# Performance work log

Measured on AMD Instinct MI355X. Metric: run time of the kernel, lower is better.

## Reference

```python
import jax, jax.numpy as jnp
import numpy as np

D_MODEL = 1024
NUM_HEADS = 16
D_K = D_MODEL // NUM_HEADS


def setup_inputs() -> dict:
    key = jax.random.key(0)
    ks = jax.random.split(key, 5)
    sd = np.sqrt(2.0 / (D_MODEL + D_MODEL))
    x = jax.random.normal(ks[0], (2, 2048, D_MODEL), dtype=jnp.float32)
    # weights stored as [out_features, in_features] like torch Linear
    w_q = jax.random.normal(ks[1], (D_MODEL, D_MODEL), dtype=jnp.float32) * (sd * sd)
    w_k = jax.random.normal(ks[2], (D_MODEL, D_MODEL), dtype=jnp.float32) * (sd * sd)
    w_v = jax.random.normal(ks[3], (D_MODEL, D_MODEL), dtype=jnp.float32) * (sd * sd)
    w_o = jax.random.normal(ks[4], (D_MODEL, D_MODEL), dtype=jnp.float32) * (sd * sd)
    return {"x": x, "w_q": w_q, "w_k": w_k, "w_v": w_v, "w_o": w_o}


def reference(x, w_q, w_k, w_v, w_o):
    B, S, D = x.shape
    H, Dk = NUM_HEADS, D_K
    # projections: x @ W.T
    q = (x @ w_q.T).reshape(B, S, H, Dk).transpose(0, 2, 1, 3)  # [B,H,S,Dk]
    k = (x @ w_k.T).reshape(B, S, H, Dk).transpose(0, 2, 1, 3)
    v = (x @ w_v.T).reshape(B, S, H, Dk).transpose(0, 2, 1, 3)
    scale = 1.0 / np.sqrt(Dk).astype(np.float32)
    scores = jnp.einsum('bhqd,bhkd->bhqk', q, k) * scale  # [B,H,S,S]
    causal = jnp.tril(jnp.ones((S, S), dtype=bool))
    scores = jnp.where(causal, scores, -jnp.inf)
    weights = jax.nn.softmax(scores, axis=-1)
    attn = jnp.einsum('bhqk,bhkd->bhqd', weights, v)  # [B,H,S,Dk]
    attn = attn.transpose(0, 2, 1, 3).reshape(B, S, D)
    return attn @ w_o.T
```

## Files before the change

kernel.cpp:

```cpp
#include <hip/hip_runtime.h>

typedef __attribute__((ext_vector_type(8))) short short8;
typedef __attribute__((ext_vector_type(4))) float f32x4;
typedef __attribute__((ext_vector_type(16))) float f32x16;
typedef __attribute__((ext_vector_type(2))) unsigned int u32x2;

#define DM 1024
#define SL 2048
#define NH 16
#define DKH 64
#define NB 2

__device__ __forceinline__ unsigned short f2bf(float f) {
    union { float f; unsigned int u; } a; a.f = f;
    unsigned int r = a.u + 0x7FFFu + ((a.u >> 16) & 1u);
    return (unsigned short)(r >> 16);
}

__device__ __forceinline__ void gl_lds16(const void* g, void* l) {
    __builtin_amdgcn_global_load_lds(
        (__attribute__((address_space(1))) void*)(g),
        (__attribute__((address_space(3))) void*)(l), 16, 0, 0);
}

__device__ __forceinline__ unsigned int cvtpk_bf16(float lo, float hi) {
    unsigned int r;
    asm("v_cvt_pk_bf16_f32 %0, %1, %2" : "=v"(r) : "v"(lo), "v"(hi));
    return r;
}

__device__ __forceinline__ void pl32swap(unsigned int &a, unsigned int &b) {
    u32x2 r = __builtin_amdgcn_permlane32_swap(a, b, false, false);
    a = r[0]; b = r[1];
}
__device__ __forceinline__ void pl32swapf(float &a, float &b) {
    unsigned int ua = __float_as_uint(a), ub = __float_as_uint(b);
    pl32swap(ua, ub);
    a = __uint_as_float(ua); b = __uint_as_float(ub);
}

__global__ __launch_bounds__(256) void convert_kernel(
    const float* __restrict__ x,  const float* __restrict__ wq,
    const float* __restrict__ wk, const float* __restrict__ wv,
    const float* __restrict__ wo,
    unsigned short* __restrict__ xb,  unsigned short* __restrict__ wqb,
    unsigned short* __restrict__ wkb, unsigned short* __restrict__ wvb,
    unsigned short* __restrict__ wob)
{
    const int NX = NB * SL * DM;
    const int NW = DM * DM;
    int t4 = (blockIdx.x * 256 + threadIdx.x) * 4;
    const float* src; unsigned short* dst; int off; float scale = 1.0f;
    if (t4 < NX)              { src = x;  dst = xb;  off = t4; }
    else if (t4 < NX + NW)    { src = wq; dst = wqb; off = t4 - NX; scale = 0.125f * 1.44269504088896f; }
    else if (t4 < NX + 2*NW)  { src = wk; dst = wkb; off = t4 - NX - NW; }
    else if (t4 < NX + 3*NW)  { src = wv; dst = wvb; off = t4 - NX - 2*NW; }
    else                      { src = wo; dst = wob; off = t4 - NX - 3*NW; }
    float4 v = *(const float4*)(src + off);
    unsigned long long p =
        (unsigned long long)f2bf(v.x * scale)
      | ((unsigned long long)f2bf(v.y * scale) << 16)
      | ((unsigned long long)f2bf(v.z * scale) << 32)
      | ((unsigned long long)f2bf(v.w * scale) << 48);
    *(unsigned long long*)(dst + off) = p;
}

__global__ __launch_bounds__(256) void gemm_bt(
    const unsigned short* __restrict__ A,
    const unsigned short* __restrict__ Bw,
    unsigned short* __restrict__ oq, unsigned short* __restrict__ ok,
    unsigned short* __restrict__ ov)
{
    __shared__ __align__(16) unsigned short As[128 * 64];
    __shared__ __align__(16) unsigned short Bs[128 * 64];
    const int tid  = threadIdx.x;
    const int lane = tid & 63;
    const int wave = tid >> 6;
    const int wm = (wave >> 1) * 64, wn = (wave & 1) * 64;
    const int bx = blockIdx.x, by = blockIdx.y;
    const int c    = lane & 15;
    const int kg16 = (lane >> 4) * 16;
    const int swz  = (c & 7) << 4;

    f32x4 acc[4][4];
    #pragma unroll
    for (int i = 0; i < 4; i++)
        #pragma unroll
        for (int j = 0; j < 4; j++) acc[i][j] = (f32x4){0.f, 0.f, 0.f, 0.f};

    const char* Ab = (const char*)A  + by * 128 * (DM * 2);
    const char* Bb = (const char*)Bw + bx * 128 * (DM * 2);

    for (int k0 = 0; k0 < DM; k0 += 64) {
        #pragma unroll
        for (int i = 0; i < 4; i++) {
            int o  = i * 4096 + tid * 16;
            int r  = o >> 7;
            int cb = o & 127;
            int src = r * (DM * 2) + k0 * 2 + (cb ^ ((r & 7) << 4));
            gl_lds16(Ab + src, (char*)As + o);
            gl_lds16(Bb + src, (char*)Bs + o);
        }
        __syncthreads();
        #pragma unroll
        for (int kk = 0; kk < 2; kk++) {
            short8 a[4], bfr[4];
            #pragma unroll
            for (int mi = 0; mi < 4; mi++)
                a[mi] = *(const short8*)((const char*)As
                        + (wm + mi * 16 + c) * 128 + ((kk * 64 + kg16) ^ swz));
            #pragma unroll
            for (int ni = 0; ni < 4; ni++)
                bfr[ni] = *(const short8*)((const char*)Bs
                        + (wn + ni * 16 + c) * 128 + ((kk * 64 + kg16) ^ swz));
            #pragma unroll
            for (int mi = 0; mi < 4; mi++)
                #pragma unroll
                for (int ni = 0; ni < 4; ni++)
                    acc[mi][ni] = __builtin_amdgcn_mfma_f32_16x16x32_bf16(
                        a[mi], bfr[ni], acc[mi][ni], 0, 0, 0);
        }
        __syncthreads();
    }

    const int r4 = (lane >> 4) * 4;
    const int mat = (bx * 128) >> 10;
    unsigned short* outb = (mat == 0) ? oq : (mat == 1) ? ok : ov;
    const int nb = bx * 128 - (mat << 10);
    #pragma unroll
    for (int mi = 0; mi < 4; mi++) {
        int m_g = by * 128 + wm + mi * 16 + r4;
        int b_  = m_g >> 11, s_ = m_g & 2047;
        #pragma unroll
        for (int ni = 0; ni < 4; ni++) {
            int n_l = nb + wn + ni * 16 + c;
            int h = n_l >> 6, dk = n_l & 63;
            #pragma unroll
            for (int j = 0; j < 4; j++)
                outb[((b_ * NH + h) * SL + (s_ + j)) * DKH + dk] = f2bf(acc[mi][ni][j]);
        }
    }
}

__global__ __launch_bounds__(256) void gemm_o(
    const unsigned short* __restrict__ A,
    const unsigned short* __restrict__ Bw,
    float* __restrict__ of)
{
    __shared__ __align__(16) unsigned short As[64 * 64];
    __shared__ __align__(16) unsigned short Bs[128 * 64];
    const int tid  = threadIdx.x;
    const int lane = tid & 63;
    const int wave = tid >> 6;
    const int wm = (wave >> 1) * 32, wn = (wave & 1) * 64;
    const int bx = blockIdx.x, by = blockIdx.y;
    const int c    = lane & 15;
    const int kg16 = (lane >> 4) * 16;
    const int swz  = (c & 7) << 4;

    f32x4 acc[2][4];
    #pragma unroll
    for (int i = 0; i < 2; i++)
        #pragma unroll
        for (int j = 0; j < 4; j++) acc[i][j] = (f32x4){0.f, 0.f, 0.f, 0.f};

    const char* Ab = (const char*)A  + by * 64  * (DM * 2);
    const char* Bb = (const char*)Bw + bx * 128 * (DM * 2);

    for (int k0 = 0; k0 < DM; k0 += 64) {
        #pragma unroll
        for (int i = 0; i < 2; i++) {
            int o  = i * 4096 + tid * 16;
            int r  = o >> 7, cb = o & 127;
            int src = r * (DM * 2) + k0 * 2 + (cb ^ ((r & 7) << 4));
            gl_lds16(Ab + src, (char*)As + o);
        }
        #pragma unroll
        for (int i = 0; i < 4; i++) {
            int o  = i * 4096 + tid * 16;
            int r  = o >> 7, cb = o & 127;
            int src = r * (DM * 2) + k0 * 2 + (cb ^ ((r & 7) << 4));
            gl_lds16(Bb + src, (char*)Bs + o);
        }
        __syncthreads();
        #pragma unroll
        for (int kk = 0; kk < 2; kk++) {
            short8 a[2], bfr[4];
            #pragma unroll
            for (int mi = 0; mi < 2; mi++)
                a[mi] = *(const short8*)((const char*)As
                        + (wm + mi * 16 + c) * 128 + ((kk * 64 + kg16) ^ swz));
            #pragma unroll
            for (int ni = 0; ni < 4; ni++)
                bfr[ni] = *(const short8*)((const char*)Bs
                        + (wn + ni * 16 + c) * 128 + ((kk * 64 + kg16) ^ swz));
            #pragma unroll
            for (int mi = 0; mi < 2; mi++)
                #pragma unroll
                for (int ni = 0; ni < 4; ni++)
                    acc[mi][ni] = __builtin_amdgcn_mfma_f32_16x16x32_bf16(
                        a[mi], bfr[ni], acc[mi][ni], 0, 0, 0);
        }
        __syncthreads();
    }

    const int r4 = (lane >> 4) * 4;
    #pragma unroll
    for (int mi = 0; mi < 2; mi++) {
        int m_g = by * 64 + wm + mi * 16 + r4;
        #pragma unroll
        for (int ni = 0; ni < 4; ni++) {
            int n_g = bx * 128 + wn + ni * 16 + c;
            #pragma unroll
            for (int j = 0; j < 4; j++)
                of[(m_g + j) * DM + n_g] = acc[mi][ni][j];
        }
    }
}

__global__ __launch_bounds__(128) void attn_kernel(
    const unsigned short* __restrict__ Q,
    const unsigned short* __restrict__ K,
    const unsigned short* __restrict__ V,
    unsigned short* __restrict__ O,
    unsigned short* __restrict__ partO,
    float* __restrict__ ml)
{
    __shared__ __align__(16) unsigned short Kl[64 * 64];
    __shared__ __align__(16) unsigned short Vt[8 * 64 * 8];
    const int tid = threadIdx.x, lane = tid & 63, wave = tid >> 6;
    const int ln31 = lane & 31, hi = lane >> 5;
    const int m  = blockIdx.x >> 5;
    const int bh = blockIdx.x & 31;
    const int rr = m >> 3, g = m & 7;
    int item;
    if (rr < 2)       item = m;
    else if (rr == 2) item = 16 + g;
    else if (rr == 3) item = 31 - g;
    else if (rr == 4) item = 32 + g;
    else              item = 47 - g;
    int qt, cch, t0, ntc;
    if (item < 16)      { qt = 16 + item;              cch = 0; t0 = 0;  ntc = 16; }
    else if (item < 32) { int j = item - 16; qt = 31 - j; cch = 1; t0 = 16; ntc = 16 - j; }
    else                { int j = item - 32; qt = 15 - j; cch = 0; t0 = 0;  ntc = 16 - j; }
    const int b = bh >> 4, h = bh & 15;
    const int bhi = b * NH + h;
    const unsigned short* Qg = Q + bhi * (SL * DKH);
    const unsigned short* Kg = K + bhi * (SL * DKH);
    const unsigned short* Vg = V + bhi * (SL * DKH);
    const int qw = qt * 64 + wave * 32;
    const int vd0 = (tid & 31) * 2, c0 = tid >> 5;

    short8 qf[4];
    #pragma unroll
    for (int ks = 0; ks < 4; ks++)
        qf[ks] = *(const short8*)&Qg[(qw + ln31) * DKH + ks * 16 + hi * 8];

    f32x16 OT0, OT1;
    #pragma unroll
    for (int r = 0; r < 16; r++) { OT0[r] = 0.f; OT1[r] = 0.f; }
    float mrun = -1e30f, ls = 0.f;

    short8 kreg[4];
    unsigned int vreg[16];


    {
        const size_t kvb = (size_t)t0 * 64;
        #pragma unroll
        for (int i = 0; i < 4; i++) {
            int s = i * 128 + tid;
            int kv = s >> 3, k8 = s & 7;
            kreg[i] = *(const short8*)&Kg[(kvb + kv) * DKH + k8 * 8];
        }
        #pragma unroll
        for (int c2 = 0; c2 < 2; c2++)
            #pragma unroll
            for (int i = 0; i < 8; i++)
                vreg[c2 * 8 + i] = *(const unsigned int*)&Vg[(kvb + (c0 + 4 * c2) * 8 + i) * DKH + vd0];
        #pragma unroll
        for (int i = 0; i < 4; i++) {
            int s = i * 128 + tid;
            int kv = s >> 3, k8 = (s & 7) ^ (kv & 7);
            *(short8*)((char*)Kl + kv * 128 + k8 * 16) = kreg[i];
        }
        #pragma unroll
        for (int c2 = 0; c2 < 2; c2++) {
            int chunk = c0 + 4 * c2;
            short8 sa, sb;
            #pragma unroll
            for (int i = 0; i < 8; i++) {
                unsigned int pr = vreg[c2 * 8 + i];
                sa[i] = (short)(pr & 0xFFFFu);
                sb[i] = (short)(pr >> 16);
            }
            *(short8*)&Vt[(chunk * 64 + vd0) * 8]     = sa;
            *(short8*)&Vt[(chunk * 64 + vd0 + 1) * 8] = sb;
        }
        __syncthreads();
    }

    for (int tt = 0; tt < ntc; ++tt) {
        const int t = t0 + tt;
        const int kv0 = t * 64;

        if (tt + 1 < ntc) {
            const size_t kv1 = (size_t)(t + 1) * 64;
            #pragma unroll
            for (int i = 0; i < 4; i++) {
                int s = i * 128 + tid;
                int kv = s >> 3, k8 = s & 7;
                kreg[i] = *(const short8*)&Kg[(kv1 + kv) * DKH + k8 * 8];
            }
            #pragma unroll
            for (int c2 = 0; c2 < 2; c2++)
                #pragma unroll
                for (int i = 0; i < 8; i++)
                    vreg[c2 * 8 + i] = *(const unsigned int*)&Vg[(kv1 + (c0 + 4 * c2) * 8 + i) * DKH + vd0];
        }

        f32x16 S0, S1;
        #pragma unroll
        for (int r = 0; r < 16; r++) { S0[r] = 0.f; S1[r] = 0.f; }
        __builtin_amdgcn_s_setprio(1);
        #pragma unroll
        for (int ks = 0; ks < 4; ks++) {
            int ko = (ks * 32 + hi * 16) ^ ((ln31 & 7) << 4);
            short8 ka0 = *(const short8*)((const char*)Kl + ln31 * 128 + ko);
            short8 ka1 = *(const short8*)((const char*)Kl + (32 + ln31) * 128 + ko);
            S0 = __builtin_amdgcn_mfma_f32_32x32x16_bf16(ka0, qf[ks], S0, 0, 0, 0);
            S1 = __builtin_amdgcn_mfma_f32_32x32x16_bf16(ka1, qf[ks], S1, 0, 0, 0);
        }
        __builtin_amdgcn_s_setprio(0);

        if (t == qt) {
            const int qrel0 = qw + ln31 - kv0 - 4 * hi;
            const int qrel1 = qrel0 - 32;
            #pragma unroll
            for (int r = 0; r < 16; r++) {
                const int ro = (r & 3) + 8 * (r >> 2);
                if (ro > qrel0) S0[r] = -1e30f;
                if (ro > qrel1) S1[r] = -1e30f;
            }
        }

        float mx = fmaxf(S0[0], S1[0]);
        #pragma unroll
        for (int r = 1; r < 16; r++) mx = fmaxf(mx, fmaxf(S0[r], S1[r]));
        float ma = mx, mb = mx;
        pl32swapf(ma, mb);
        float rm = fmaxf(ma, mb);

        if (__any(rm > mrun + 8.f)) {
            float nm = fmaxf(mrun, rm);
            float corr = __builtin_amdgcn_exp2f(mrun - nm);
            mrun = nm; ls *= corr;
            #pragma unroll
            for (int r = 0; r < 16; r++) { OT0[r] *= corr; OT1[r] *= corr; }
        }

        float psum = 0.f;
        #pragma unroll
        for (int r = 0; r < 16; r++) {
            S0[r] = __builtin_amdgcn_exp2f(S0[r] - mrun); psum += S0[r];
            S1[r] = __builtin_amdgcn_exp2f(S1[r] - mrun); psum += S1[r];
        }
        ls += psum;

        short8 pf[4];
        {
            unsigned int wa, wb, wc, wd;
            wa = cvtpk_bf16(S0[0], S0[1]);   wb = cvtpk_bf16(S0[4], S0[5]);
            pl32swap(wa, wb);
            wc = cvtpk_bf16(S0[2], S0[3]);   wd = cvtpk_bf16(S0[6], S0[7]);
            pl32swap(wc, wd);
            union { unsigned int u[4]; short8 s; } w0 = {{wa, wc, wb, wd}};
            pf[0] = w0.s;

            wa = cvtpk_bf16(S0[8], S0[9]);   wb = cvtpk_bf16(S0[12], S0[13]);
            pl32swap(wa, wb);
            wc = cvtpk_bf16(S0[10], S0[11]); wd = cvtpk_bf16(S0[14], S0[15]);
            pl32swap(wc, wd);
            union { unsigned int u[4]; short8 s; } w1 = {{wa, wc, wb, wd}};
            pf[1] = w1.s;

            wa = cvtpk_bf16(S1[0], S1[1]);   wb = cvtpk_bf16(S1[4], S1[5]);
            pl32swap(wa, wb);
            wc = cvtpk_bf16(S1[2], S1[3]);   wd = cvtpk_bf16(S1[6], S1[7]);
            pl32swap(wc, wd);
            union { unsigned int u[4]; short8 s; } w2 = {{wa, wc, wb, wd}};
            pf[2] = w2.s;

            wa = cvtpk_bf16(S1[8], S1[9]);   wb = cvtpk_bf16(S1[12], S1[13]);
            pl32swap(wa, wb);
            wc = cvtpk_bf16(S1[10], S1[11]); wd = cvtpk_bf16(S1[14], S1[15]);
            pl32swap(wc, wd);
            union { unsigned int u[4]; short8 s; } w3 = {{wa, wc, wb, wd}};
            pf[3] = w3.s;
        }

        __builtin_amdgcn_s_setprio(1);
        #pragma unroll
        for (int ks2 = 0; ks2 < 4; ks2++) {
            int slot = (ks2 * 2 + hi) * 64;
            short8 va0 = *(const short8*)&Vt[(slot + ln31) * 8];
            short8 va1 = *(const short8*)&Vt[(slot + 32 + ln31) * 8];
            OT0 = __builtin_amdgcn_mfma_f32_32x32x16_bf16(va0, pf[ks2], OT0, 0, 0, 0);
            OT1 = __builtin_amdgcn_mfma_f32_32x32x16_bf16(va1, pf[ks2], OT1, 0, 0, 0);
        }
        __builtin_amdgcn_s_setprio(0);

        if (tt + 1 < ntc) {
            __syncthreads();
            #pragma unroll
            for (int i = 0; i < 4; i++) {
                int s = i * 128 + tid;
                int kv = s >> 3, k8 = (s & 7) ^ (kv & 7);
                *(short8*)((char*)Kl + kv * 128 + k8 * 16) = kreg[i];
            }
            #pragma unroll
            for (int c2 = 0; c2 < 2; c2++) {
                int chunk = c0 + 4 * c2;
                short8 sa, sb;
                #pragma unroll
                for (int i = 0; i < 8; i++) {
                    unsigned int pr = vreg[c2 * 8 + i];
                    sa[i] = (short)(pr & 0xFFFFu);
                    sb[i] = (short)(pr >> 16);
                }
                *(short8*)&Vt[(chunk * 64 + vd0) * 8]     = sa;
                *(short8*)&Vt[(chunk * 64 + vd0 + 1) * 8] = sb;
            }
            __syncthreads();
        }
    }

    float la = ls, lb = ls;
    pl32swapf(la, lb);
    const float lrow = la + lb;
    const int qrow_l = wave * 32 + ln31;
    if (qt >= 16) {
        const int rec = (bh * 16 + (qt - 16)) * 2 + cch;
        unsigned short* po = partO + (size_t)rec * 4096;
        if (hi == 0) {
            ml[(rec * 64 + qrow_l) * 2]     = mrun;
            ml[(rec * 64 + qrow_l) * 2 + 1] = lrow;
        }
        #pragma unroll
        for (int r = 0; r < 16; r++) {
            const int d0 = (r & 3) + 8 * (r >> 2) + 4 * hi;
            po[qrow_l * 64 + d0]      = f2bf(OT0[r]);
            po[qrow_l * 64 + 32 + d0] = f2bf(OT1[r]);
        }
    } else {
        float inv = 1.0f / lrow;
        const int qrow = qw + ln31;
        const size_t base = (size_t)(b * SL + qrow) * DM + h * DKH;
        #pragma unroll
        for (int r = 0; r < 16; r++) {
            const int d0 = (r & 3) + 8 * (r >> 2) + 4 * hi;
            O[base + d0]      = f2bf(OT0[r] * inv);
            O[base + 32 + d0] = f2bf(OT1[r] * inv);
        }
    }
}

__global__ __launch_bounds__(256) void combine_kernel(
    const unsigned short* __restrict__ partO,
    const float* __restrict__ ml,
    unsigned short* __restrict__ O)
{
    const int gi = blockIdx.x * 8 + (threadIdx.x >> 5);
    const int ln = threadIdx.x & 31;
    const int bh = gi >> 10, rem = gi & 1023;
    const int qtl = rem >> 6, row = rem & 63;
    const int qt = 16 + qtl;
    const int rec0 = (bh * 16 + qtl) * 2;
    const float m0 = ml[(rec0 * 64 + row) * 2];
    const float l0 = ml[(rec0 * 64 + row) * 2 + 1];
    const float m1 = ml[((rec0 + 1) * 64 + row) * 2];
    const float l1 = ml[((rec0 + 1) * 64 + row) * 2 + 1];
    const float M  = fmaxf(m0, m1);
    const float w0 = exp2f(m0 - M), w1 = exp2f(m1 - M);
    const float inv = 1.0f / (w0 * l0 + w1 * l1);
    const unsigned int u0 = *(const unsigned int*)&partO[(size_t)rec0 * 4096 + row * 64 + ln * 2];
    const unsigned int u1 = *(const unsigned int*)&partO[(size_t)(rec0 + 1) * 4096 + row * 64 + ln * 2];
    const float a0 = __uint_as_float(u0 << 16);
    const float b0 = __uint_as_float(u0 & 0xFFFF0000u);
    const float a1 = __uint_as_float(u1 << 16);
    const float b1 = __uint_as_float(u1 & 0xFFFF0000u);
    const float oa = (a0 * w0 + a1 * w1) * inv;
    const float ob = (b0 * w0 + b1 * w1) * inv;
    const unsigned int pack = (unsigned int)f2bf(oa) | ((unsigned int)f2bf(ob) << 16);
    const int b = bh >> 4, h = bh & 15;
    const size_t base = (size_t)(b * SL + qt * 64 + row) * DM + h * DKH;
    *(unsigned int*)&O[base + ln * 2] = pack;
}

extern "C" void kernel_launch(void* const* d_in, const int* in_sizes, int n_in,
                              void* d_out, int out_size, void* d_ws, size_t ws_size,
                              hipStream_t stream)
{
    const float* x  = (const float*)d_in[0];
    const float* wq = (const float*)d_in[1];
    const float* wk = (const float*)d_in[2];
    const float* wv = (const float*)d_in[3];
    const float* wo = (const float*)d_in[4];
    char* ws = (char*)d_ws;
    unsigned short* xb  = (unsigned short*)(ws);
    unsigned short* wqb = (unsigned short*)(ws + (8ll  << 20));
    unsigned short* wkb = (unsigned short*)(ws + (10ll << 20));
    unsigned short* wvb = (unsigned short*)(ws + (12ll << 20));
    unsigned short* wob = (unsigned short*)(ws + (14ll << 20));
    unsigned short* Qb  = (unsigned short*)(ws + (16ll << 20));
    unsigned short* Kb  = (unsigned short*)(ws + (24ll << 20));
    unsigned short* Vb  = (unsigned short*)(ws + (32ll << 20));
    unsigned short* Abf = (unsigned short*)(ws + (40ll << 20));
    unsigned short* partO = (unsigned short*)(ws);
    float*          mlbuf = (float*)(ws + (8ll << 20));
    float* out = (float*)d_out;

    convert_kernel<<<dim3(8192), dim3(256), 0, stream>>>(
        x, wq, wk, wv, wo, xb, wqb, wkb, wvb, wob);

    gemm_bt<<<dim3(24, 32), dim3(256), 0, stream>>>(xb, wqb, Qb, Kb, Vb);

    attn_kernel<<<dim3(1536), dim3(128), 0, stream>>>(Qb, Kb, Vb, Abf, partO, mlbuf);
    combine_kernel<<<dim3(4096), dim3(256), 0, stream>>>(partO, mlbuf, Abf);

    gemm_o<<<dim3(8, 64), dim3(256), 0, stream>>>(Abf, wob, out);
}
```

Baseline: 110.3 us.

## Use persistent atomic work queue for attention with finer causal splits and double-buffered K/V

```diff
diff --git a/kernel.cpp b/kernel.cpp
--- a/kernel.cpp
+++ b/kernel.cpp
@@ -10,6 +10,7 @@
 #define NH 16
 #define DKH 64
 #define NB 2
+#define NITEMS 1792
 
 __device__ __forceinline__ unsigned short f2bf(float f) {
     union { float f; unsigned int u; } a; a.f = f;
@@ -69,8 +70,9 @@
     const unsigned short* __restrict__ A,
     const unsigned short* __restrict__ Bw,
     unsigned short* __restrict__ oq, unsigned short* __restrict__ ok,
-    unsigned short* __restrict__ ov)
+    unsigned short* __restrict__ ov, unsigned int* __restrict__ counter)
 {
+    if (blockIdx.x == 0 && blockIdx.y == 0 && threadIdx.x == 0) *counter = 0u;
     __shared__ __align__(16) unsigned short As[128 * 64];
     __shared__ __align__(16) unsigned short Bs[128 * 64];
     const int tid  = threadIdx.x;
@@ -224,200 +226,72 @@
     const unsigned short* __restrict__ V,
     unsigned short* __restrict__ O,
     unsigned short* __restrict__ partO,
-    float* __restrict__ ml)
+    float* __restrict__ ml,
+    unsigned int* __restrict__ counter)
 {
-    __shared__ __align__(16) unsigned short Kl[64 * 64];
-    __shared__ __align__(16) unsigned short Vt[8 * 64 * 8];
+    __shared__ __align__(16) unsigned short Kl[2][64 * 64];
+    __shared__ __align__(16) unsigned short Vt[2][8 * 64 * 8];
+    __shared__ int s_item;
     const int tid = threadIdx.x, lane = tid & 63, wave = tid >> 6;
     const int ln31 = lane & 31, hi = lane >> 5;
-    const int m  = blockIdx.x >> 5;
-    const int bh = blockIdx.x & 31;
-    const int rr = m >> 3, g = m & 7;
-    int item;
-    if (rr < 2)       item = m;
-    else if (rr == 2) item = 16 + g;
-    else if (rr == 3) item = 31 - g;
-    else if (rr == 4) item = 32 + g;
-    else              item = 47 - g;
-    int qt, cch, t0, ntc;
-    if (item < 16)      { qt = 16 + item;              cch = 0; t0 = 0;  ntc = 16; }
-    else if (item < 32) { int j = item - 16; qt = 31 - j; cch = 1; t0 = 16; ntc = 16 - j; }
-    else                { int j = item - 32; qt = 15 - j; cch = 0; t0 = 0;  ntc = 16 - j; }
-    const int b = bh >> 4, h = bh & 15;
-    const int bhi = b * NH + h;
-    const unsigned short* Qg = Q + bhi * (SL * DKH);
-    const unsigned short* Kg = K + bhi * (SL * DKH);
-    const unsigned short* Vg = V + bhi * (SL * DKH);
-    const int qw = qt * 64 + wave * 32;
     const int vd0 = (tid & 31) * 2, c0 = tid >> 5;
 
-    short8 qf[4];
-    #pragma unroll
-    for (int ks = 0; ks < 4; ks++)
-        qf[ks] = *(const short8*)&Qg[(qw + ln31) * DKH + ks * 16 + hi * 8];
-
-    f32x16 OT0, OT1;
-    #pragma unroll
-    for (int r = 0; r < 16; r++) { OT0[r] = 0.f; OT1[r] = 0.f; }
-    float mrun = -1e30f, ls = 0.f;
-
-    short8 kreg[4];
-    unsigned int vreg[16];
-
-
-    {
-        const size_t kvb = (size_t)t0 * 64;
-        #pragma unroll
-        for (int i = 0; i < 4; i++) {
-            int s = i * 128 + tid;
-            int kv = s >> 3, k8 = s & 7;
-            kreg[i] = *(const short8*)&Kg[(kvb + kv) * DKH + k8 * 8];
-        }
-        #pragma unroll
-        for (int c2 = 0; c2 < 2; c2++)
-            #pragma unroll
-            for (int i = 0; i < 8; i++)
-                vreg[c2 * 8 + i] = *(const unsigned int*)&Vg[(kvb + (c0 + 4 * c2) * 8 + i) * DKH + vd0];
-        #pragma unroll
-        for (int i = 0; i < 4; i++) {
-            int s = i * 128 + tid;
-            int kv = s >> 3, k8 = (s & 7) ^ (kv & 7);
-            *(short8*)((char*)Kl + kv * 128 + k8 * 16) = kreg[i];
-        }
-        #pragma unroll
-        for (int c2 = 0; c2 < 2; c2++) {
-            int chunk = c0 + 4 * c2;
-            short8 sa, sb;
-            #pragma unroll
-            for (int i = 0; i < 8; i++) {
-                unsigned int pr = vreg[c2 * 8 + i];
-                sa[i] = (short)(pr & 0xFFFFu);
-                sb[i] = (short)(pr >> 16);
-            }
-            *(short8*)&Vt[(chunk * 64 + vd0) * 8]     = sa;
-            *(short8*)&Vt[(chunk * 64 + vd0 + 1) * 8] = sb;
-        }
+    for (;;) {
+        if (tid == 0) s_item = (int)atomicAdd(counter, 1u);
         __syncthreads();
-    }
-
-    for (int tt = 0; tt < ntc; ++tt) {
-        const int t = t0 + tt;
-        const int kv0 = t * 64;
-
-        if (tt + 1 < ntc) {
-            const size_t kv1 = (size_t)(t + 1) * 64;
+        const int it = s_item;
+        if (it >= NITEMS) break;
+
+        const int bh = it & 31;
+        const int w  = it >> 5;
+        int qt, t0, ntc, cch;
+        if (w < 48) {
+            qt = 31 - (w >> 1); cch = w & 1;
+            const int h0 = (qt + 2) >> 1;
+            t0 = cch ? h0 : 0; ntc = cch ? (qt + 1 - h0) : h0;
+        } else {
+            qt = 55 - w; cch = 0; t0 = 0; ntc = qt + 1;
+        }
+        const int b = bh >> 4, h = bh & 15;
+        const int bhi = b * NH + h;
+        const unsigned short* Qg = Q + bhi * (SL * DKH);
+        const unsigned short* Kg = K + bhi * (SL * DKH);
+        const unsigned short* Vg = V + bhi * (SL * DKH);
+        const int qw = qt * 64 + wave * 32;
+
+        short8 qf[4];
+        #pragma unroll
+        for (int ks = 0; ks < 4; ks++)
+            qf[ks] = *(const short8*)&Qg[(qw + ln31) * DKH + ks * 16 + hi * 8];
+
+        f32x16 OT0, OT1;
+        #pragma unroll
+        for (int r = 0; r < 16; r++) { OT0[r] = 0.f; OT1[r] = 0.f; }
+        float mrun = -1e30f, ls = 0.f;
+
+        unsigned int vreg[16];
+
+        {
+            const size_t kvb = (size_t)t0 * 64;
             #pragma unroll
             for (int i = 0; i < 4; i++) {
                 int s = i * 128 + tid;
-                int kv = s >> 3, k8 = s & 7;
-                kreg[i] = *(const short8*)&Kg[(kv1 + kv) * DKH + k8 * 8];
+                int kv = s >> 3;
+                int k8 = (s & 7) ^ (kv & 7);
+                gl_lds16((const char*)Kg + (kvb + kv) * 128 + k8 * 16,
+                         (char*)&Kl[0][0] + s * 16);
             }
             #pragma unroll
             for (int c2 = 0; c2 < 2; c2++)
                 #pragma unroll
                 for (int i = 0; i < 8; i++)
-                    vreg[c2 * 8 + i] = *(const unsigned int*)&Vg[(kv1 + (c0 + 4 * c2) * 8 + i) * DKH + vd0];
-        }
-
-        f32x16 S0, S1;
-        #pragma unroll
-        for (int r = 0; r < 16; r++) { S0[r] = 0.f; S1[r] = 0.f; }
-        __builtin_amdgcn_s_setprio(1);
-        #pragma unroll
-        for (int ks = 0; ks < 4; ks++) {
-            int ko = (ks * 32 + hi * 16) ^ ((ln31 & 7) << 4);
-            short8 ka0 = *(const short8*)((const char*)Kl + ln31 * 128 + ko);
-            short8 ka1 = *(const short8*)((const char*)Kl + (32 + ln31) * 128 + ko);
-            S0 = __builtin_amdgcn_mfma_f32_32x32x16_bf16(ka0, qf[ks], S0, 0, 0, 0);
-            S1 = __builtin_amdgcn_mfma_f32_32x32x16_bf16(ka1, qf[ks], S1, 0, 0, 0);
-        }
-        __builtin_amdgcn_s_setprio(0);
-
-        if (t == qt) {
-            const int qrel0 = qw + ln31 - kv0 - 4 * hi;
-            const int qrel1 = qrel0 - 32;
-            #pragma unroll
-            for (int r = 0; r < 16; r++) {
-                const int ro = (r & 3) + 8 * (r >> 2);
-                if (ro > qrel0) S0[r] = -1e30f;
-                if (ro > qrel1) S1[r] = -1e30f;
-            }
-        }
-
-        float mx = fmaxf(S0[0], S1[0]);
-        #pragma unroll
-        for (int r = 1; r < 16; r++) mx = fmaxf(mx, fmaxf(S0[r], S1[r]));
-        float ma = mx, mb = mx;
-        pl32swapf(ma, mb);
-        float rm = fmaxf(ma, mb);
-
-        if (__any(rm > mrun + 8.f)) {
-            float nm = fmaxf(mrun, rm);
-            float corr = __builtin_amdgcn_exp2f(mrun - nm);
-            mrun = nm; ls *= corr;
-            #pragma unroll
-            for (int r = 0; r < 16; r++) { OT0[r] *= corr; OT1[r] *= corr; }
-        }
-
-        float psum = 0.f;
-        #pragma unroll
-        for (int r = 0; r < 16; r++) {
-            S0[r] = __builtin_amdgcn_exp2f(S0[r] - mrun); psum += S0[r];
-            S1[r] = __builtin_amdgcn_exp2f(S1[r] - mrun); psum += S1[r];
-        }
-        ls += psum;
-
-        short8 pf[4];
-        {
-            unsigned int wa, wb, wc, wd;
-            wa = cvtpk_bf16(S0[0], S0[1]);   wb = cvtpk_bf16(S0[4], S0[5]);
-            pl32swap(wa, wb);
-            wc = cvtpk_bf16(S0[2], S0[3]);   wd = cvtpk_bf16(S0[6], S0[7]);
-            pl32swap(wc, wd);
-            union { unsigned int u[4]; short8 s; } w0 = {{wa, wc, wb, wd}};
-            pf[0] = w0.s;
-
-            wa = cvtpk_bf16(S0[8], S0[9]);   wb = cvtpk_bf16(S0[12], S0[13]);
-            pl32swap(wa, wb);
-            wc = cvtpk_bf16(S0[10], S0[11]); wd = cvtpk_bf16(S0[14], S0[15]);
-            pl32swap(wc, wd);
-            union { unsigned int u[4]; short8 s; } w1 = {{wa, wc, wb, wd}};
-            pf[1] = w1.s;
-
-            wa = cvtpk_bf16(S1[0], S1[1]);   wb = cvtpk_bf16(S1[4], S1[5]);
-            pl32swap(wa, wb);
-            wc = cvtpk_bf16(S1[2], S1[3]);   wd = cvtpk_bf16(S1[6], S1[7]);
-            pl32swap(wc, wd);
-            union { unsigned int u[4]; short8 s; } w2 = {{wa, wc, wb, wd}};
-            pf[2] = w2.s;
-
-            wa = cvtpk_bf16(S1[8], S1[9]);   wb = cvtpk_bf16(S1[12], S1[13]);
-            pl32swap(wa, wb);
-            wc = cvtpk_bf16(S1[10], S1[11]); wd = cvtpk_bf16(S1[14], S1[15]);
-            pl32swap(wc, wd);
-            union { unsigned int u[4]; short8 s; } w3 = {{wa, wc, wb, wd}};
-            pf[3] = w3.s;
-        }
-
-        __builtin_amdgcn_s_setprio(1);
-        #pragma unroll
-        for (int ks2 = 0; ks2 < 4; ks2++) {
-            int slot = (ks2 * 2 + hi) * 64;
-            short8 va0 = *(const short8*)&Vt[(slot + ln31) * 8];
-            short8 va1 = *(const short8*)&Vt[(slot + 32 + ln31) * 8];
-            OT0 = __builtin_amdgcn_mfma_f32_32x32x16_bf16(va0, pf[ks2], OT0, 0, 0, 0);
-            OT1 = __builtin_amdgcn_mfma_f32_32x32x16_bf16(va1, pf[ks2], OT1, 0, 0, 0);
-        }
-        __builtin_amdgcn_s_setprio(0);
-
-        if (tt + 1 < ntc) {
-            __syncthreads();
-            #pragma unroll
-            for (int i = 0; i < 4; i++) {
-                int s = i * 128 + tid;
-                int kv = s >> 3, k8 = (s & 7) ^ (kv & 7);
-                *(short8*)((char*)Kl + kv * 128 + k8 * 16) = kreg[i];
-            }
+                    vreg[c2 * 8 + i] = *(const unsigned int*)&Vg[(kvb + (c0 + 4 * c2) * 8 + i) * DKH + vd0];
+        }
+
+        for (int tt = 0; tt < ntc; ++tt) {
+            const int t = t0 + tt;
+            const int buf = tt & 1;
+            const int kv0 = t * 64;
             #pragma unroll
             for (int c2 = 0; c2 < 2; c2++) {
                 int chunk = c0 + 4 * c2;
@@ -428,39 +302,159 @@
                     sa[i] = (short)(pr & 0xFFFFu);
                     sb[i] = (short)(pr >> 16);
                 }
-                *(short8*)&Vt[(chunk * 64 + vd0) * 8]     = sa;
-                *(short8*)&Vt[(chunk * 64 + vd0 + 1) * 8] = sb;
+                *(short8*)&Vt[buf][(chunk * 64 + vd0) * 8]     = sa;
+                *(short8*)&Vt[buf][(chunk * 64 + vd0 + 1) * 8] = sb;
             }
             __syncthreads();
-        }
-    }
-
-    float la = ls, lb = ls;
-    pl32swapf(la, lb);
-    const float lrow = la + lb;
-    const int qrow_l = wave * 32 + ln31;
-    if (qt >= 16) {
-        const int rec = (bh * 16 + (qt - 16)) * 2 + cch;
-        unsigned short* po = partO + (size_t)rec * 4096;
-        if (hi == 0) {
-            ml[(rec * 64 + qrow_l) * 2]     = mrun;
-            ml[(rec * 64 + qrow_l) * 2 + 1] = lrow;
-        }
-        #pragma unroll
-        for (int r = 0; r < 16; r++) {
-            const int d0 = (r & 3) + 8 * (r >> 2) + 4 * hi;
-            po[qrow_l * 64 + d0]      = f2bf(OT0[r]);
-            po[qrow_l * 64 + 32 + d0] = f2bf(OT1[r]);
-        }
-    } else {
-        float inv = 1.0f / lrow;
-        const int qrow = qw + ln31;
-        const size_t base = (size_t)(b * SL + qrow) * DM + h * DKH;
-        #pragma unroll
-        for (int r = 0; r < 16; r++) {
-            const int d0 = (r & 3) + 8 * (r >> 2) + 4 * hi;
-            O[base + d0]      = f2bf(OT0[r] * inv);
-            O[base + 32 + d0] = f2bf(OT1[r] * inv);
+
+            if (tt + 1 < ntc) {
+                const size_t kv1 = (size_t)(t + 1) * 64;
+                #pragma unroll
+                for (int i = 0; i < 4; i++) {
+                    int s = i * 128 + tid;
+                    int kv = s >> 3;
+                    int k8 = (s & 7) ^ (kv & 7);
+                    gl_lds16((const char*)Kg + (kv1 + kv) * 128 + k8 * 16,
+                             (char*)&Kl[buf ^ 1][0] + s * 16);
+                }
+                #pragma unroll
+                for (int c2 = 0; c2 < 2; c2++)
+                    #pragma unroll
+                    for (int i = 0; i < 8; i++)
+                        vreg[c2 * 8 + i] = *(const unsigned int*)&Vg[(kv1 + (c0 + 4 * c2) * 8 + i) * DKH + vd0];
+            }
+
+            const char* kb = (const char*)&Kl[buf][0];
+            const unsigned short* vb = &Vt[buf][0];
+
+            f32x16 S0, S1;
+            #pragma unroll
+            for (int r = 0; r < 16; r++) { S0[r] = 0.f; S1[r] = 0.f; }
+            __builtin_amdgcn_s_setprio(1);
+            #pragma unroll
+            for (int ks = 0; ks < 4; ks++) {
+                int ko = (ks * 32 + hi * 16) ^ ((ln31 & 7) << 4);
+                short8 ka0 = *(const short8*)(kb + ln31 * 128 + ko);
+                short8 ka1 = *(const short8*)(kb + (32 + ln31) * 128 + ko);
+                S0 = __builtin_amdgcn_mfma_f32_32x32x16_bf16(ka0, qf[ks], S0, 0, 0, 0);
+                S1 = __builtin_amdgcn_mfma_f32_32x32x16_bf16(ka1, qf[ks], S1, 0, 0, 0);
+            }
+            __builtin_amdgcn_s_setprio(0);
+
+            if (t == qt) {
+                const int qrel0 = qw + ln31 - kv0 - 4 * hi;
+                const int qrel1 = qrel0 - 32;
+                #pragma unroll
+                for (int r = 0; r < 16; r++) {
+                    const int ro = (r & 3) + 8 * (r >> 2);
+                    if (ro > qrel0) S0[r] = -1e30f;
+                    if (ro > qrel1) S1[r] = -1e30f;
+                }
+            }
+
+            float mt[8];
+            #pragma unroll
+            for (int r = 0; r < 8; r++)
+                mt[r] = fmaxf(fmaxf(S0[r], S0[r + 8]), fmaxf(S1[r], S1[r + 8]));
+            float mx = fmaxf(fmaxf(fmaxf(mt[0], mt[1]), fmaxf(mt[2], mt[3])),
+                             fmaxf(fmaxf(mt[4], mt[5]), fmaxf(mt[6], mt[7])));
+            float ma = mx, mb = mx;
+            pl32swapf(ma, mb);
+            float rm = fmaxf(ma, mb);
+
+            if (__any(rm > mrun + 8.f)) {
+                float nm = fmaxf(mrun, rm);
+                float corr = __builtin_amdgcn_exp2f(mrun - nm);
+                mrun = nm; ls *= corr;
+                #pragma unroll
+                for (int r = 0; r < 16; r++) { OT0[r] *= corr; OT1[r] *= corr; }
+            }
+
+            float ps0 = 0.f, ps1 = 0.f, ps2 = 0.f, ps3 = 0.f;
+            #pragma unroll
+            for (int r = 0; r < 16; r += 4) {
+                S0[r]     = __builtin_amdgcn_exp2f(S0[r]     - mrun); ps0 += S0[r];
+                S0[r + 1] = __builtin_amdgcn_exp2f(S0[r + 1] - mrun); ps1 += S0[r + 1];
+                S0[r + 2] = __builtin_amdgcn_exp2f(S0[r + 2] - mrun); ps2 += S0[r + 2];
+                S0[r + 3] = __builtin_amdgcn_exp2f(S0[r + 3] - mrun); ps3 += S0[r + 3];
+                S1[r]     = __builtin_amdgcn_exp2f(S1[r]     - mrun); ps0 += S1[r];
+                S1[r + 1] = __builtin_amdgcn_exp2f(S1[r + 1] - mrun); ps1 += S1[r + 1];
+                S1[r + 2] = __builtin_amdgcn_exp2f(S1[r + 2] - mrun); ps2 += S1[r + 2];
+                S1[r + 3] = __builtin_amdgcn_exp2f(S1[r + 3] - mrun); ps3 += S1[r + 3];
+            }
+            ls += (ps0 + ps1) + (ps2 + ps3);
+
+            short8 pf[4];
+            {
+                unsigned int wa, wb, wc, wd;
+                wa = cvtpk_bf16(S0[0], S0[1]);   wb = cvtpk_bf16(S0[4], S0[5]);
+                pl32swap(wa, wb);
+                wc = cvtpk_bf16(S0[2], S0[3]);   wd = cvtpk_bf16(S0[6], S0[7]);
+                pl32swap(wc, wd);
+                union { unsigned int u[4]; short8 s; } w0 = {{wa, wc, wb, wd}};
+                pf[0] = w0.s;
+
+                wa = cvtpk_bf16(S0[8], S0[9]);   wb = cvtpk_bf16(S0[12], S0[13]);
+                pl32swap(wa, wb);
+                wc = cvtpk_bf16(S0[10], S0[11]); wd = cvtpk_bf16(S0[14], S0[15]);
+                pl32swap(wc, wd);
+                union { unsigned int u[4]; short8 s; } w1 = {{wa, wc, wb, wd}};
+                pf[1] = w1.s;
+
+                wa = cvtpk_bf16(S1[0], S1[1]);   wb = cvtpk_bf16(S1[4], S1[5]);
+                pl32swap(wa, wb);
+                wc = cvtpk_bf16(S1[2], S1[3]);   wd = cvtpk_bf16(S1[6], S1[7]);
+                pl32swap(wc, wd);
+                union { unsigned int u[4]; short8 s; } w2 = {{wa, wc, wb, wd}};
+                pf[2] = w2.s;
+
+                wa = cvtpk_bf16(S1[8], S1[9]);   wb = cvtpk_bf16(S1[12], S1[13]);
+                pl32swap(wa, wb);
+                wc = cvtpk_bf16(S1[10], S1[11]); wd = cvtpk_bf16(S1[14], S1[15]);
+                pl32swap(wc, wd);
+                union { unsigned int u[4]; short8 s; } w3 = {{wa, wc, wb, wd}};
+                pf[3] = w3.s;
+            }
+
+            __builtin_amdgcn_s_setprio(1);
+            #pragma unroll
+            for (int ks2 = 0; ks2 < 4; ks2++) {
+                int slot = (ks2 * 2 + hi) * 64;
+                short8 va0 = *(const short8*)&vb[(slot + ln31) * 8];
+                short8 va1 = *(const short8*)&vb[(slot + 32 + ln31) * 8];
+                OT0 = __builtin_amdgcn_mfma_f32_32x32x16_bf16(va0, pf[ks2], OT0, 0, 0, 0);
+                OT1 = __builtin_amdgcn_mfma_f32_32x32x16_bf16(va1, pf[ks2], OT1, 0, 0, 0);
+            }
+            __builtin_amdgcn_s_setprio(0);
+        }
+
+        float la = ls, lb = ls;
+        pl32swapf(la, lb);
+        const float lrow = la + lb;
+        const int qrow_l = wave * 32 + ln31;
+        if (w < 48) {
+            const int rec = (bh * 24 + (31 - qt)) * 2 + cch;
+            unsigned short* po = partO + (size_t)rec * 4096;
+            if (hi == 0) {
+                ml[(rec * 64 + qrow_l) * 2]     = mrun;
+                ml[(rec * 64 + qrow_l) * 2 + 1] = lrow;
+            }
+            #pragma unroll
+            for (int r = 0; r < 16; r++) {
+                const int d0 = (r & 3) + 8 * (r >> 2) + 4 * hi;
+                po[qrow_l * 64 + d0]      = f2bf(OT0[r]);
+                po[qrow_l * 64 + 32 + d0] = f2bf(OT1[r]);
+            }
+        } else {
+            float inv = 1.0f / lrow;
+            const int qrow = qw + ln31;
+            const size_t base = (size_t)(b * SL + qrow) * DM + h * DKH;
+            #pragma unroll
+            for (int r = 0; r < 16; r++) {
+                const int d0 = (r & 3) + 8 * (r >> 2) + 4 * hi;
+                O[base + d0]      = f2bf(OT0[r] * inv);
+                O[base + 32 + d0] = f2bf(OT1[r] * inv);
+            }
         }
     }
 }
@@ -472,10 +466,10 @@
 {
     const int gi = blockIdx.x * 8 + (threadIdx.x >> 5);
     const int ln = threadIdx.x & 31;
-    const int bh = gi >> 10, rem = gi & 1023;
-    const int qtl = rem >> 6, row = rem & 63;
-    const int qt = 16 + qtl;
-    const int rec0 = (bh * 16 + qtl) * 2;
+    const int bh = gi / 1536, rem = gi - bh * 1536;
+    const int qi = rem >> 6, row = rem & 63;
+    const int qt = 31 - qi;
+    const int rec0 = (bh * 24 + qi) * 2;
     const float m0 = ml[(rec0 * 64 + row) * 2];
     const float l0 = ml[(rec0 * 64 + row) * 2 + 1];
     const float m1 = ml[((rec0 + 1) * 64 + row) * 2];
@@ -517,16 +511,18 @@
     unsigned short* Vb  = (unsigned short*)(ws + (32ll << 20));
     unsigned short* Abf = (unsigned short*)(ws + (40ll << 20));
     unsigned short* partO = (unsigned short*)(ws);
-    float*          mlbuf = (float*)(ws + (8ll << 20));
+    float*          mlbuf   = (float*)(ws + (12ll << 20));
+    unsigned int*   counter = (unsigned int*)(ws + (13ll << 20) + (512ll << 10));
     float* out = (float*)d_out;
 
     convert_kernel<<<dim3(8192), dim3(256), 0, stream>>>(
         x, wq, wk, wv, wo, xb, wqb, wkb, wvb, wob);
 
-    gemm_bt<<<dim3(24, 32), dim3(256), 0, stream>>>(xb, wqb, Qb, Kb, Vb);
-
-    attn_kernel<<<dim3(1536), dim3(128), 0, stream>>>(Qb, Kb, Vb, Abf, partO, mlbuf);
-    combine_kernel<<<dim3(4096), dim3(256), 0, stream>>>(partO, mlbuf, Abf);
+    gemm_bt<<<dim3(24, 32), dim3(256), 0, stream>>>(xb, wqb, Qb, Kb, Vb, counter);
+
+    attn_kernel<<<dim3(1280), dim3(128), 0, stream>>>(
+        Qb, Kb, Vb, Abf, partO, mlbuf, counter);
+    combine_kernel<<<dim3(6144), dim3(256), 0, stream>>>(partO, mlbuf, Abf);
 
     gemm_o<<<dim3(8, 64), dim3(256), 0, stream>>>(Abf, wob, out);
 }
```

New measurement: 127.6 us. +15.7%, slower.

## Double-buffer K/V LDS tiles with direct global-to-LDS K loads

Applied to the files above, without the earlier changes.

```diff
diff --git a/kernel.cpp b/kernel.cpp
--- a/kernel.cpp
+++ b/kernel.cpp
@@ -226,19 +226,12 @@
     unsigned short* __restrict__ partO,
     float* __restrict__ ml)
 {
-    __shared__ __align__(16) unsigned short Kl[64 * 64];
-    __shared__ __align__(16) unsigned short Vt[8 * 64 * 8];
+    __shared__ __align__(16) unsigned short Kl[2][64 * 64];
+    __shared__ __align__(16) unsigned short Vt[2][8 * 64 * 8];
     const int tid = threadIdx.x, lane = tid & 63, wave = tid >> 6;
     const int ln31 = lane & 31, hi = lane >> 5;
-    const int m  = blockIdx.x >> 5;
-    const int bh = blockIdx.x & 31;
-    const int rr = m >> 3, g = m & 7;
-    int item;
-    if (rr < 2)       item = m;
-    else if (rr == 2) item = 16 + g;
-    else if (rr == 3) item = 31 - g;
-    else if (rr == 4) item = 32 + g;
-    else              item = 47 - g;
+    const int item = blockIdx.x >> 5;
+    const int bh   = blockIdx.x & 31;
     int qt, cch, t0, ntc;
     if (item < 16)      { qt = 16 + item;              cch = 0; t0 = 0;  ntc = 16; }
     else if (item < 32) { int j = item - 16; qt = 31 - j; cch = 1; t0 = 16; ntc = 16 - j; }
@@ -261,29 +254,29 @@
     for (int r = 0; r < 16; r++) { OT0[r] = 0.f; OT1[r] = 0.f; }
     float mrun = -1e30f, ls = 0.f;
 
-    short8 kreg[4];
     unsigned int vreg[16];
-
 
     {
         const size_t kvb = (size_t)t0 * 64;
         #pragma unroll
         for (int i = 0; i < 4; i++) {
             int s = i * 128 + tid;
-            int kv = s >> 3, k8 = s & 7;
-            kreg[i] = *(const short8*)&Kg[(kvb + kv) * DKH + k8 * 8];
+            int kv = s >> 3;
+            int k8 = (s & 7) ^ (kv & 7);
+            gl_lds16((const char*)Kg + (kvb + kv) * 128 + k8 * 16,
+                     (char*)&Kl[0][0] + s * 16);
         }
         #pragma unroll
         for (int c2 = 0; c2 < 2; c2++)
             #pragma unroll
             for (int i = 0; i < 8; i++)
                 vreg[c2 * 8 + i] = *(const unsigned int*)&Vg[(kvb + (c0 + 4 * c2) * 8 + i) * DKH + vd0];
-        #pragma unroll
-        for (int i = 0; i < 4; i++) {
-            int s = i * 128 + tid;
-            int kv = s >> 3, k8 = (s & 7) ^ (kv & 7);
-            *(short8*)((char*)Kl + kv * 128 + k8 * 16) = kreg[i];
-        }
+    }
+
+    for (int tt = 0; tt < ntc; ++tt) {
+        const int t = t0 + tt;
+        const int buf = tt & 1;
+        const int kv0 = t * 64;
         #pragma unroll
         for (int c2 = 0; c2 < 2; c2++) {
             int chunk = c0 + 4 * c2;
@@ -294,23 +287,20 @@
                 sa[i] = (short)(pr & 0xFFFFu);
                 sb[i] = (short)(pr >> 16);
             }
-            *(short8*)&Vt[(chunk * 64 + vd0) * 8]     = sa;
-            *(short8*)&Vt[(chunk * 64 + vd0 + 1) * 8] = sb;
+            *(short8*)&Vt[buf][(chunk * 64 + vd0) * 8]     = sa;
+            *(short8*)&Vt[buf][(chunk * 64 + vd0 + 1) * 8] = sb;
         }
         __syncthreads();
-    }
-
-    for (int tt = 0; tt < ntc; ++tt) {
-        const int t = t0 + tt;
-        const int kv0 = t * 64;
 
         if (tt + 1 < ntc) {
             const size_t kv1 = (size_t)(t + 1) * 64;
             #pragma unroll
             for (int i = 0; i < 4; i++) {
                 int s = i * 128 + tid;
-                int kv = s >> 3, k8 = s & 7;
-                kreg[i] = *(const short8*)&Kg[(kv1 + kv) * DKH + k8 * 8];
+                int kv = s >> 3;
+                int k8 = (s & 7) ^ (kv & 7);
+                gl_lds16((const char*)Kg + (kv1 + kv) * 128 + k8 * 16,
+                         (char*)&Kl[buf ^ 1][0] + s * 16);
             }
             #pragma unroll
             for (int c2 = 0; c2 < 2; c2++)
@@ -319,6 +309,9 @@
                     vreg[c2 * 8 + i] = *(const unsigned int*)&Vg[(kv1 + (c0 + 4 * c2) * 8 + i) * DKH + vd0];
         }
 
+        const char* kb = (const char*)&Kl[buf][0];
+        const unsigned short* vb = &Vt[buf][0];
+
         f32x16 S0, S1;
         #pragma unroll
         for (int r = 0; r < 16; r++) { S0[r] = 0.f; S1[r] = 0.f; }
@@ -326,8 +319,8 @@
         #pragma unroll
         for (int ks = 0; ks < 4; ks++) {
             int ko = (ks * 32 + hi * 16) ^ ((ln31 & 7) << 4);
-            short8 ka0 = *(const short8*)((const char*)Kl + ln31 * 128 + ko);
-            short8 ka1 = *(const short8*)((const char*)Kl + (32 + ln31) * 128 + ko);
+            short8 ka0 = *(const short8*)(kb + ln31 * 128 + ko);
+            short8 ka1 = *(const short8*)(kb + (32 + ln31) * 128 + ko);
             S0 = __builtin_amdgcn_mfma_f32_32x32x16_bf16(ka0, qf[ks], S0, 0, 0, 0);
             S1 = __builtin_amdgcn_mfma_f32_32x32x16_bf16(ka1, qf[ks], S1, 0, 0, 0);
         }
@@ -403,36 +396,12 @@
         #pragma unroll
         for (int ks2 = 0; ks2 < 4; ks2++) {
             int slot = (ks2 * 2 + hi) * 64;
-            short8 va0 = *(const short8*)&Vt[(slot + ln31) * 8];
-            short8 va1 = *(const short8*)&Vt[(slot + 32 + ln31) * 8];
+            short8 va0 = *(const short8*)&vb[(slot + ln31) * 8];
+            short8 va1 = *(const short8*)&vb[(slot + 32 + ln31) * 8];
             OT0 = __builtin_amdgcn_mfma_f32_32x32x16_bf16(va0, pf[ks2], OT0, 0, 0, 0);
             OT1 = __builtin_amdgcn_mfma_f32_32x32x16_bf16(va1, pf[ks2], OT1, 0, 0, 0);
         }
         __builtin_amdgcn_s_setprio(0);
-
-        if (tt + 1 < ntc) {
-            __syncthreads();
-            #pragma unroll
-            for (int i = 0; i < 4; i++) {
-                int s = i * 128 + tid;
-                int kv = s >> 3, k8 = (s & 7) ^ (kv & 7);
-                *(short8*)((char*)Kl + kv * 128 + k8 * 16) = kreg[i];
-            }
-            #pragma unroll
-            for (int c2 = 0; c2 < 2; c2++) {
-                int chunk = c0 + 4 * c2;
-                short8 sa, sb;
-                #pragma unroll
-                for (int i = 0; i < 8; i++) {
-                    unsigned int pr = vreg[c2 * 8 + i];
-                    sa[i] = (short)(pr & 0xFFFFu);
-                    sb[i] = (short)(pr >> 16);
-                }
-                *(short8*)&Vt[(chunk * 64 + vd0) * 8]     = sa;
-                *(short8*)&Vt[(chunk * 64 + vd0 + 1) * 8] = sb;
-            }
-            __syncthreads();
-        }
     }
 
     float la = ls, lb = ls;
```

After: 104.8 us. -4.9%, faster.
